# Optimization experiments

Measured on AMD Instinct MI355X. Metric: run time of the kernel, lower is better.

## Reference

```python
import jax, jax.numpy as jnp
import numpy as np

# Module constants (from init_kwargs)
P = 10000          # query points
G = 6400           # gaussians
C = 18             # semantic classes
H, W, D = 200, 200, 16
GRID = 0.5
SCALE_MULT = 3.0
PC_MIN = jnp.array([-50.0, -50.0, -5.0], dtype=jnp.float32)
COV_IDX = np.array([0, 4, 8, 1, 5, 2])  # xx, yy, zz, xy, yz, xz of flattened 3x3


def setup_inputs() -> dict:
    key = jax.random.key(0)
    k1, k2, k3, k4, k5, k6 = jax.random.split(key, 6)
    extent = jnp.array([H, W, D], jnp.float32) * GRID  # [100, 100, 8] meters
    eps = 1e-3  # keep strictly inside grid so int voxel coords are in-range
    pts = PC_MIN + jax.random.uniform(k1, (1, P, 3), jnp.float32) * (extent - eps)
    means3D = PC_MIN + jax.random.uniform(k2, (1, G, 3), jnp.float32) * (extent - eps)
    opacities = jax.random.uniform(k3, (1, G), jnp.float32)
    semantics = jax.random.normal(k4, (1, G, C), jnp.float32)
    # scales in [0.2, 1.0] m -> radii = ceil(max_scale*3/0.5) >= 2 (assert radii >= 1)
    scales = 0.2 + 0.8 * jax.random.uniform(k5, (1, G, 3), jnp.float32)
    # cov3D is the (symmetric PD) precision matrix: R diag(1/s^2) R^T
    A = jax.random.normal(k6, (1, G, 3, 3), jnp.float32)
    Q, _ = jnp.linalg.qr(A)
    inv_var = 1.0 / (scales ** 2)
    cov3D = jnp.einsum('bgij,bgj,bgkj->bgik', Q, inv_var, Q)
    return dict(pts=pts, means3D=means3D, opacities=opacities,
                semantics=semantics, scales=scales, cov3D=cov3D)


def reference(pts, means3D, opacities, semantics, scales, cov3D):
    # squeeze batch dim (module asserts batch == 1)
    p = pts[0]                     # [P,3]
    mu = means3D[0]                # [G,3]
    op = opacities[0]              # [G]
    sem = semantics[0]             # [G,C]
    sc = scales[0]                 # [G,3]
    cov = cov3D[0].reshape(G, 9)[:, COV_IDX]  # [G,6]: xx,yy,zz,xy,yz,xz

    # integer voxel coords (cast truncates; coords are non-negative in-range)
    p_int = ((p - PC_MIN) / GRID).astype(jnp.int32)                              # [P,3]
    m_int = ((jax.lax.stop_gradient(mu) - PC_MIN) / GRID).astype(jnp.int32)      # [G,3]
    radii = jnp.ceil(sc.max(-1) * SCALE_MULT / GRID).astype(jnp.int32)           # [G]

    # voxel-box test: point voxel within per-axis radius of gaussian voxel
    mask = (jnp.abs(p_int[:, None, :] - m_int[None, :, :]) <= radii[None, :, None]).all(-1)  # [P,G]

    # Mahalanobis power with precision matrix entries
    d = p[:, None, :] - mu[None, :, :]           # [P,G,3]
    dx, dy, dz = d[..., 0], d[..., 1], d[..., 2]
    power = (-0.5 * (cov[None, :, 0] * dx * dx
                     + cov[None, :, 1] * dy * dy
                     + cov[None, :, 2] * dz * dz)
             - cov[None, :, 3] * dx * dy
             - cov[None, :, 4] * dy * dz
             - cov[None, :, 5] * dx * dz)        # [P,G]

    w = jnp.where(mask, jnp.exp(power) * op[None, :], 0.0)  # [P,G]
    logits = w @ sem                                         # [P,C]
    return logits
```

## Files before the change

kernel.cpp:

```cpp
#include <hip/hip_runtime.h>
#include <math.h>

#define P_TOTAL 10000
#define G_TOTAL 6400
#define C_CLS   18
#define CS_SH   3
#define NCX     25
#define NCELL   (NCX * NCX)
#define BCAP    256
#define PCAP    96
#define NTHR    512

__global__ void __launch_bounds__(NTHR)
la_cell1(const float* __restrict__ pts,
         const float* __restrict__ means3D,
         const float* __restrict__ opacities,
         const float* __restrict__ semantics,
         const float* __restrict__ scales,
         const float* __restrict__ cov3D,
         float* __restrict__ out) {
    __shared__ int4 sbox[BCAP];
    __shared__ int  splist[PCAP];
    __shared__ int  snb, snp;

    const int t = threadIdx.x;
    const int cell = blockIdx.x;
    const int ccx = cell % NCX;
    const int ccy = cell / NCX;

    if (t == 0) { snb = 0; snp = 0; }
    __syncthreads();

    for (int i = t; i < P_TOTAL; i += NTHR) {
        float px = pts[i * 3 + 0];
        float py = pts[i * 3 + 1];
        int cx = ((int)((px + 50.0f) * 2.0f)) >> CS_SH;
        int cy = ((int)((py + 50.0f) * 2.0f)) >> CS_SH;
        if (cx == ccx && cy == ccy) {
            int s = atomicAdd(&snp, 1);
            if (s < PCAP) splist[s] = i;
        }
    }

    for (int g = t; g < G_TOTAL; g += NTHR) {
        float mx = means3D[g * 3 + 0];
        float my = means3D[g * 3 + 1];
        float mz = means3D[g * 3 + 2];
        float sx = scales[g * 3 + 0];
        float sy = scales[g * 3 + 1];
        float sz = scales[g * 3 + 2];
        int mix = (int)((mx + 50.0f) * 2.0f);
        int miy = (int)((my + 50.0f) * 2.0f);
        int miz = (int)((mz + 5.0f) * 2.0f);
        int r = (int)ceilf((fmaxf(fmaxf(sx, sy), sz) * 3.0f) * 2.0f);
        int w = 2 * r;
        int minx = mix - r, miny = miy - r, minz = miz - r;
        int cx0 = max(minx, 0) >> CS_SH;
        int cx1 = min(minx + w, 199) >> CS_SH;
        int cy0 = max(miny, 0) >> CS_SH;
        int cy1 = min(miny + w, 199) >> CS_SH;
        if (ccx >= cx0 && ccx <= cx1 && ccy >= cy0 && ccy <= cy1) {
            int s = atomicAdd(&snb, 1);
            if (s < BCAP) sbox[s] = make_int4(minx, miny, minz, (w << 16) | g);
        }
    }
    __syncthreads();

    const int np = min(snp, PCAP);
    const int nb = min(snb, BCAP);
    const int wv = t >> 6, lane = t & 63;

    for (int idx = wv; idx < np; idx += NTHR / 64) {
        int pt = splist[idx];
        float px = pts[pt * 3 + 0];
        float py = pts[pt * 3 + 1];
        float pz = pts[pt * 3 + 2];
        int pix = (int)((px + 50.0f) * 2.0f);
        int piy = (int)((py + 50.0f) * 2.0f);
        int piz = (int)((pz + 5.0f) * 2.0f);

        float acc = 0.0f;
        for (int base = 0; base < nb; base += 64) {
            int i = base + lane;
            float wgt = 0.0f;
            int gid = 0;
            if (i < nb) {
                int4 b = sbox[i];
                unsigned w  = ((unsigned)b.w) >> 16;
                unsigned ux = (unsigned)(pix - b.x);
                unsigned uy = (unsigned)(piy - b.y);
                unsigned uz = (unsigned)(piz - b.z);
                if (ux <= w && uy <= w && uz <= w) {
                    gid = b.w & 0xffff;
                    float mx = means3D[gid * 3 + 0];
                    float my = means3D[gid * 3 + 1];
                    float mz = means3D[gid * 3 + 2];
                    const float* cv = cov3D + (size_t)gid * 9;
                    float dx = px - mx, dy = py - my, dz = pz - mz;
                    float pw = -0.5f * (cv[0] * dx * dx + cv[4] * dy * dy + cv[8] * dz * dz)
                               - cv[1] * dx * dy - cv[5] * dy * dz - cv[2] * dx * dz;
                    wgt = __expf(pw) * opacities[gid];
                }
            }
            unsigned long long m = __ballot(wgt != 0.0f);
            while (m) {
                int h = (int)__builtin_ctzll(m);
                m &= m - 1;
                float wh = __shfl(wgt, h, 64);
                int   gh = __shfl(gid, h, 64);
                if (lane < C_CLS)
                    acc = fmaf(wh, semantics[(size_t)gh * C_CLS + lane], acc);
            }
        }

        if (lane < C_CLS)
            out[(size_t)pt * C_CLS + lane] = acc;
    }
}

extern "C" void kernel_launch(void* const* d_in, const int* in_sizes, int n_in,
                              void* d_out, int out_size, void* d_ws, size_t ws_size,
                              hipStream_t stream) {
    const float* pts      = (const float*)d_in[0];
    const float* means3D  = (const float*)d_in[1];
    const float* opac     = (const float*)d_in[2];
    const float* sem      = (const float*)d_in[3];
    const float* scales   = (const float*)d_in[4];
    const float* cov3D    = (const float*)d_in[5];
    float* out = (float*)d_out;

    la_cell1<<<NCELL, NTHR, 0, stream>>>(pts, means3D, opac, sem, scales, cov3D, out);
}
```

Baseline: 31.02 us.

## Bin points and gaussians globally once, with a grid-wide barrier before per-cell compute

Before this change, every block scanned all points and all gaussians to find the ones in its own cell. Now a single parallel pass bins points and gaussian footprints into per-cell lists in workspace using global atomics. A software grid barrier then separates binning from compute, and a persistent grid of 256 blocks loops over the 625 cells. The semantic accumulation also batches 16 ballot hits per pass to expose memory-level parallelism. The costs are a memset launch, global atomic contention, and a spin barrier that relies on all blocks being co-resident. PCAP also drops to 64, which could truncate points in dense cells.

```diff
diff --git a/kernel.cpp b/kernel.cpp
--- a/kernel.cpp
+++ b/kernel.cpp
@@ -7,42 +7,48 @@
 #define CS_SH   3
 #define NCX     25
 #define NCELL   (NCX * NCX)
-#define BCAP    256
-#define PCAP    96
-#define NTHR    512
+#define MAXE    256
+#define PCAP    64
+#define NBLK    256
+#define NTHR    256
+#define HB      16
 
-__global__ void __launch_bounds__(NTHR)
-la_cell1(const float* __restrict__ pts,
-         const float* __restrict__ means3D,
-         const float* __restrict__ opacities,
-         const float* __restrict__ semantics,
-         const float* __restrict__ scales,
-         const float* __restrict__ cov3D,
-         float* __restrict__ out) {
-    __shared__ int4 sbox[BCAP];
-    __shared__ int  splist[PCAP];
-    __shared__ int  snb, snp;
+#define OFF_BAR    0
+#define OFF_CNT    64
+#define OFF_PCNT   4096
+#define OFF_PLIST  8192
+#define OFF_ENT    (8192 + NCELL * PCAP * 4)
+
+__global__ void __launch_bounds__(NTHR, 4)
+la_bar(const float* __restrict__ pts,
+       const float* __restrict__ means3D,
+       const float* __restrict__ opacities,
+       const float* __restrict__ semantics,
+       const float* __restrict__ scales,
+       const float* __restrict__ cov3D,
+       char* __restrict__ ws,
+       float* __restrict__ out) {
+    int*  bar     = (int*)(ws + OFF_BAR);
+    int*  counts  = (int*)(ws + OFF_CNT);
+    int*  pcnt    = (int*)(ws + OFF_PCNT);
+    int*  plist   = (int*)(ws + OFF_PLIST);
+    int4* entries = (int4*)(ws + OFF_ENT);
 
     const int t = threadIdx.x;
-    const int cell = blockIdx.x;
-    const int ccx = cell % NCX;
-    const int ccy = cell / NCX;
+    const int gtid = blockIdx.x * NTHR + t;
 
-    if (t == 0) { snb = 0; snp = 0; }
-    __syncthreads();
-
-    for (int i = t; i < P_TOTAL; i += NTHR) {
-        float px = pts[i * 3 + 0];
-        float py = pts[i * 3 + 1];
+    if (gtid < P_TOTAL) {
+        float px = pts[gtid * 3 + 0];
+        float py = pts[gtid * 3 + 1];
         int cx = ((int)((px + 50.0f) * 2.0f)) >> CS_SH;
         int cy = ((int)((py + 50.0f) * 2.0f)) >> CS_SH;
-        if (cx == ccx && cy == ccy) {
-            int s = atomicAdd(&snp, 1);
-            if (s < PCAP) splist[s] = i;
-        }
+        int cell = cy * NCX + cx;
+        int s = atomicAdd(&pcnt[cell], 1);
+        if (s < PCAP) plist[cell * PCAP + s] = gtid;
     }
 
-    for (int g = t; g < G_TOTAL; g += NTHR) {
+    if (gtid < G_TOTAL) {
+        int g = gtid;
         float mx = means3D[g * 3 + 0];
         float my = means3D[g * 3 + 1];
         float mz = means3D[g * 3 + 2];
@@ -59,62 +65,95 @@
         int cx1 = min(minx + w, 199) >> CS_SH;
         int cy0 = max(miny, 0) >> CS_SH;
         int cy1 = min(miny + w, 199) >> CS_SH;
-        if (ccx >= cx0 && ccx <= cx1 && ccy >= cy0 && ccy <= cy1) {
-            int s = atomicAdd(&snb, 1);
-            if (s < BCAP) sbox[s] = make_int4(minx, miny, minz, (w << 16) | g);
+        int4 e = make_int4(minx, miny, minz, (w << 16) | g);
+        for (int cy = cy0; cy <= cy1; ++cy) {
+            for (int cx = cx0; cx <= cx1; ++cx) {
+                int cell = cy * NCX + cx;
+                int s = atomicAdd(&counts[cell], 1);
+                if (s < MAXE) entries[(size_t)cell * MAXE + s] = e;
+            }
         }
     }
+
+    __threadfence();
     __syncthreads();
+    if (t == 0) {
+        atomicAdd(&bar[0], 1);
+        while (atomicAdd(&bar[0], 0) < NBLK)
+            __builtin_amdgcn_s_sleep(8);
+    }
+    __syncthreads();
+    __threadfence();
 
-    const int np = min(snp, PCAP);
-    const int nb = min(snb, BCAP);
+    __shared__ int4 sbox[MAXE];
+    __shared__ int  spl[PCAP];
     const int wv = t >> 6, lane = t & 63;
 
-    for (int idx = wv; idx < np; idx += NTHR / 64) {
-        int pt = splist[idx];
-        float px = pts[pt * 3 + 0];
-        float py = pts[pt * 3 + 1];
-        float pz = pts[pt * 3 + 2];
-        int pix = (int)((px + 50.0f) * 2.0f);
-        int piy = (int)((py + 50.0f) * 2.0f);
-        int piz = (int)((pz + 5.0f) * 2.0f);
+    for (int cell = blockIdx.x; cell < NCELL; cell += NBLK) {
+        int nb = min(counts[cell], MAXE);
+        int np = min(pcnt[cell], PCAP);
+        __syncthreads();
+        for (int i = t; i < nb; i += NTHR) sbox[i] = entries[(size_t)cell * MAXE + i];
+        for (int i = t; i < np; i += NTHR) spl[i] = plist[cell * PCAP + i];
+        __syncthreads();
 
-        float acc = 0.0f;
-        for (int base = 0; base < nb; base += 64) {
-            int i = base + lane;
-            float wgt = 0.0f;
-            int gid = 0;
-            if (i < nb) {
-                int4 b = sbox[i];
-                unsigned w  = ((unsigned)b.w) >> 16;
-                unsigned ux = (unsigned)(pix - b.x);
-                unsigned uy = (unsigned)(piy - b.y);
-                unsigned uz = (unsigned)(piz - b.z);
-                if (ux <= w && uy <= w && uz <= w) {
-                    gid = b.w & 0xffff;
-                    float mx = means3D[gid * 3 + 0];
-                    float my = means3D[gid * 3 + 1];
-                    float mz = means3D[gid * 3 + 2];
-                    const float* cv = cov3D + (size_t)gid * 9;
-                    float dx = px - mx, dy = py - my, dz = pz - mz;
-                    float pw = -0.5f * (cv[0] * dx * dx + cv[4] * dy * dy + cv[8] * dz * dz)
-                               - cv[1] * dx * dy - cv[5] * dy * dz - cv[2] * dx * dz;
-                    wgt = __expf(pw) * opacities[gid];
+        for (int idx = wv; idx < np; idx += NTHR / 64) {
+            int pt = spl[idx];
+            float px = pts[pt * 3 + 0];
+            float py = pts[pt * 3 + 1];
+            float pz = pts[pt * 3 + 2];
+            int pix = (int)((px + 50.0f) * 2.0f);
+            int piy = (int)((py + 50.0f) * 2.0f);
+            int piz = (int)((pz + 5.0f) * 2.0f);
+
+            float acc = 0.0f;
+            for (int base = 0; base < nb; base += 64) {
+                int i = base + lane;
+                float wgt = 0.0f;
+                int gid = 0;
+                if (i < nb) {
+                    int4 b = sbox[i];
+                    unsigned w  = ((unsigned)b.w) >> 16;
+                    unsigned ux = (unsigned)(pix - b.x);
+                    unsigned uy = (unsigned)(piy - b.y);
+                    unsigned uz = (unsigned)(piz - b.z);
+                    if (ux <= w && uy <= w && uz <= w) {
+                        gid = b.w & 0xffff;
+                        float mx = means3D[gid * 3 + 0];
+                        float my = means3D[gid * 3 + 1];
+                        float mz = means3D[gid * 3 + 2];
+                        const float* cv = cov3D + (size_t)gid * 9;
+                        float dx = px - mx, dy = py - my, dz = pz - mz;
+                        float pw = -0.5f * (cv[0] * dx * dx + cv[4] * dy * dy + cv[8] * dz * dz)
+                                   - cv[1] * dx * dy - cv[5] * dy * dz - cv[2] * dx * dz;
+                        wgt = __expf(pw) * opacities[gid];
+                    }
+                }
+                unsigned long long m = __ballot(wgt != 0.0f);
+                while (m) {
+                    float wh[HB];
+                    int   gh[HB];
+#pragma unroll
+                    for (int k = 0; k < HB; ++k) {
+                        bool has = (m != 0);
+                        int h = (int)__builtin_ctzll(m | 0x8000000000000000ULL);
+                        float w_ = __shfl(wgt, h, 64);
+                        int   g_ = __shfl(gid, h, 64);
+                        wh[k] = has ? w_ : 0.0f;
+                        gh[k] = has ? g_ : 0;
+                        m &= m - 1;
+                    }
+                    if (lane < C_CLS) {
+#pragma unroll
+                        for (int k = 0; k < HB; ++k)
+                            acc = fmaf(wh[k], semantics[(size_t)gh[k] * C_CLS + lane], acc);
+                    }
                 }
             }
-            unsigned long long m = __ballot(wgt != 0.0f);
-            while (m) {
-                int h = (int)__builtin_ctzll(m);
-                m &= m - 1;
-                float wh = __shfl(wgt, h, 64);
-                int   gh = __shfl(gid, h, 64);
-                if (lane < C_CLS)
-                    acc = fmaf(wh, semantics[(size_t)gh * C_CLS + lane], acc);
-            }
+
+            if (lane < C_CLS)
+                out[(size_t)pt * C_CLS + lane] = acc;
         }
-
-        if (lane < C_CLS)
-            out[(size_t)pt * C_CLS + lane] = acc;
     }
 }
 
@@ -128,6 +167,8 @@
     const float* scales   = (const float*)d_in[4];
     const float* cov3D    = (const float*)d_in[5];
     float* out = (float*)d_out;
+    char* ws = (char*)d_ws;
 
-    la_cell1<<<NCELL, NTHR, 0, stream>>>(pts, means3D, opac, sem, scales, cov3D, out);
+    hipMemsetAsync(ws, 0, 8192, stream);
+    la_bar<<<NBLK, NTHR, 0, stream>>>(pts, means3D, opac, sem, scales, cov3D, ws, out);
 }
```

Result: slower. 97.24 us (+213.5%).

## Prebin gaussians and points into supercells before per-cell gather

Applied to the files above, without the earlier changes.

Replaces the per-block full scan over all 10000 points and 6400 gaussians with a three-kernel pipeline. The first kernel packs gaussian voxel boxes, the second scatters gaussians and points into 5x5 supercell lists in workspace, and the gather kernel reads only its supercell's candidates. It also batches the ballot-driven semantic accumulation into groups of 16 hits so the loads can be issued together. This adds two extra kernel launches and global atomics, plus fixed capacities (768 and 640 entries per supercell) that could silently drop entries if they overflow.

```diff
diff --git a/kernel.cpp b/kernel.cpp
--- a/kernel.cpp
+++ b/kernel.cpp
@@ -7,42 +7,28 @@
 #define CS_SH   3
 #define NCX     25
 #define NCELL   (NCX * NCX)
+#define SC_DIV  5
+#define NSC     25
+#define SBCAP   768
+#define SPCAP   640
 #define BCAP    256
 #define PCAP    96
 #define NTHR    512
-
-__global__ void __launch_bounds__(NTHR)
-la_cell1(const float* __restrict__ pts,
-         const float* __restrict__ means3D,
-         const float* __restrict__ opacities,
-         const float* __restrict__ semantics,
-         const float* __restrict__ scales,
-         const float* __restrict__ cov3D,
-         float* __restrict__ out) {
-    __shared__ int4 sbox[BCAP];
-    __shared__ int  splist[PCAP];
-    __shared__ int  snb, snp;
-
-    const int t = threadIdx.x;
-    const int cell = blockIdx.x;
-    const int ccx = cell % NCX;
-    const int ccy = cell / NCX;
-
-    if (t == 0) { snb = 0; snp = 0; }
-    __syncthreads();
-
-    for (int i = t; i < P_TOTAL; i += NTHR) {
-        float px = pts[i * 3 + 0];
-        float py = pts[i * 3 + 1];
-        int cx = ((int)((px + 50.0f) * 2.0f)) >> CS_SH;
-        int cy = ((int)((py + 50.0f) * 2.0f)) >> CS_SH;
-        if (cx == ccx && cy == ccy) {
-            int s = atomicAdd(&snp, 1);
-            if (s < PCAP) splist[s] = i;
-        }
-    }
-
-    for (int g = t; g < G_TOTAL; g += NTHR) {
+#define HB      16
+
+#define OFF_BOX  0
+#define OFF_CNT  102400
+#define OFF_SBL  102656
+#define OFF_SPL  179456
+
+__global__ void la_pack(const float* __restrict__ means3D,
+                        const float* __restrict__ scales,
+                        char* __restrict__ ws) {
+    int4* boxes = (int4*)(ws + OFF_BOX);
+    int*  cnt   = (int*)(ws + OFF_CNT);
+    int tid = blockIdx.x * 256 + threadIdx.x;
+    if (tid < G_TOTAL) {
+        int g = tid;
         float mx = means3D[g * 3 + 0];
         float my = means3D[g * 3 + 1];
         float mz = means3D[g * 3 + 2];
@@ -54,14 +40,99 @@
         int miz = (int)((mz + 5.0f) * 2.0f);
         int r = (int)ceilf((fmaxf(fmaxf(sx, sy), sz) * 3.0f) * 2.0f);
         int w = 2 * r;
-        int minx = mix - r, miny = miy - r, minz = miz - r;
-        int cx0 = max(minx, 0) >> CS_SH;
-        int cx1 = min(minx + w, 199) >> CS_SH;
-        int cy0 = max(miny, 0) >> CS_SH;
-        int cy1 = min(miny + w, 199) >> CS_SH;
+        boxes[g] = make_int4(mix - r, miy - r, miz - r, (w << 16) | g);
+    } else if (tid < G_TOTAL + 64) {
+        cnt[tid - G_TOTAL] = 0;
+    }
+}
+
+__global__ void la_scat(const float* __restrict__ pts,
+                        char* __restrict__ ws) {
+    const int4* boxes = (const int4*)(ws + OFF_BOX);
+    int* cnt    = (int*)(ws + OFF_CNT);
+    int* sblist = (int*)(ws + OFF_SBL);
+    int* splist = (int*)(ws + OFF_SPL);
+    int tid = blockIdx.x * 256 + threadIdx.x;
+    if (tid < G_TOTAL * 4) {
+        int g = tid >> 2, k = tid & 3;
+        int4 b = boxes[g];
+        int w = b.w >> 16;
+        int cx0 = max(b.x, 0) >> CS_SH;
+        int cx1 = min(b.x + w, 199) >> CS_SH;
+        int cy0 = max(b.y, 0) >> CS_SH;
+        int cy1 = min(b.y + w, 199) >> CS_SH;
+        int sx0 = cx0 / SC_DIV, sx1 = cx1 / SC_DIV;
+        int sy0 = cy0 / SC_DIV, sy1 = cy1 / SC_DIV;
+        int dx = k & 1, dy = k >> 1;
+        int sx = sx0 + dx, sy = sy0 + dy;
+        if (sx <= sx1 && sy <= sy1) {
+            int sc = sy * SC_DIV + sx;
+            int s = atomicAdd(&cnt[sc], 1);
+            if (s < SBCAP) sblist[sc * SBCAP + s] = g;
+        }
+    } else if (tid < G_TOTAL * 4 + P_TOTAL) {
+        int p = tid - G_TOTAL * 4;
+        float px = pts[p * 3 + 0];
+        float py = pts[p * 3 + 1];
+        int cx = ((int)((px + 50.0f) * 2.0f)) >> CS_SH;
+        int cy = ((int)((py + 50.0f) * 2.0f)) >> CS_SH;
+        int sc = (cy / SC_DIV) * SC_DIV + (cx / SC_DIV);
+        int s = atomicAdd(&cnt[32 + sc], 1);
+        if (s < SPCAP) splist[sc * SPCAP + s] = p;
+    }
+}
+
+__global__ void __launch_bounds__(NTHR)
+la_gather(const float* __restrict__ pts,
+          const float* __restrict__ means3D,
+          const float* __restrict__ opacities,
+          const float* __restrict__ semantics,
+          const float* __restrict__ cov3D,
+          const char* __restrict__ ws,
+          float* __restrict__ out) {
+    const int4* boxes  = (const int4*)(ws + OFF_BOX);
+    const int*  cnt    = (const int*)(ws + OFF_CNT);
+    const int*  sblist = (const int*)(ws + OFF_SBL);
+    const int*  splist = (const int*)(ws + OFF_SPL);
+
+    __shared__ int4 sbox[BCAP];
+    __shared__ int  spl[PCAP];
+    __shared__ int  snb, snp;
+
+    const int t = threadIdx.x;
+    const int cell = blockIdx.x;
+    const int ccx = cell % NCX;
+    const int ccy = cell / NCX;
+    const int sc  = (ccy / SC_DIV) * SC_DIV + (ccx / SC_DIV);
+
+    if (t == 0) { snb = 0; snp = 0; }
+    __syncthreads();
+
+    const int npl = min(cnt[32 + sc], SPCAP);
+    for (int i = t; i < npl; i += NTHR) {
+        int p = splist[sc * SPCAP + i];
+        float px = pts[p * 3 + 0];
+        float py = pts[p * 3 + 1];
+        int cx = ((int)((px + 50.0f) * 2.0f)) >> CS_SH;
+        int cy = ((int)((py + 50.0f) * 2.0f)) >> CS_SH;
+        if (cx == ccx && cy == ccy) {
+            int s = atomicAdd(&snp, 1);
+            if (s < PCAP) spl[s] = p;
+        }
+    }
+
+    const int nbl = min(cnt[sc], SBCAP);
+    for (int i = t; i < nbl; i += NTHR) {
+        int g = sblist[sc * SBCAP + i];
+        int4 b = boxes[g];
+        int w = b.w >> 16;
+        int cx0 = max(b.x, 0) >> CS_SH;
+        int cx1 = min(b.x + w, 199) >> CS_SH;
+        int cy0 = max(b.y, 0) >> CS_SH;
+        int cy1 = min(b.y + w, 199) >> CS_SH;
         if (ccx >= cx0 && ccx <= cx1 && ccy >= cy0 && ccy <= cy1) {
             int s = atomicAdd(&snb, 1);
-            if (s < BCAP) sbox[s] = make_int4(minx, miny, minz, (w << 16) | g);
+            if (s < BCAP) sbox[s] = b;
         }
     }
     __syncthreads();
@@ -71,7 +142,7 @@
     const int wv = t >> 6, lane = t & 63;
 
     for (int idx = wv; idx < np; idx += NTHR / 64) {
-        int pt = splist[idx];
+        int pt = spl[idx];
         float px = pts[pt * 3 + 0];
         float py = pts[pt * 3 + 1];
         float pz = pts[pt * 3 + 2];
@@ -104,12 +175,23 @@
             }
             unsigned long long m = __ballot(wgt != 0.0f);
             while (m) {
-                int h = (int)__builtin_ctzll(m);
-                m &= m - 1;
-                float wh = __shfl(wgt, h, 64);
-                int   gh = __shfl(gid, h, 64);
-                if (lane < C_CLS)
-                    acc = fmaf(wh, semantics[(size_t)gh * C_CLS + lane], acc);
+                float wh[HB];
+                int   gh[HB];
+#pragma unroll
+                for (int k = 0; k < HB; ++k) {
+                    bool has = (m != 0);
+                    int h = (int)__builtin_ctzll(m | 0x8000000000000000ULL);
+                    float w_ = __shfl(wgt, h, 64);
+                    int   g_ = __shfl(gid, h, 64);
+                    wh[k] = has ? w_ : 0.0f;
+                    gh[k] = has ? g_ : 0;
+                    m &= m - 1;
+                }
+                if (lane < C_CLS) {
+#pragma unroll
+                    for (int k = 0; k < HB; ++k)
+                        acc = fmaf(wh[k], semantics[(size_t)gh[k] * C_CLS + lane], acc);
+                }
             }
         }
 
@@ -128,6 +210,9 @@
     const float* scales   = (const float*)d_in[4];
     const float* cov3D    = (const float*)d_in[5];
     float* out = (float*)d_out;
-
-    la_cell1<<<NCELL, NTHR, 0, stream>>>(pts, means3D, opac, sem, scales, cov3D, out);
-}
+    char* ws = (char*)d_ws;
+
+    la_pack<<<(G_TOTAL + 64 + 255) / 256, 256, 0, stream>>>(means3D, scales, ws);
+    la_scat<<<(G_TOTAL * 4 + P_TOTAL + 255) / 256, 256, 0, stream>>>(pts, ws);
+    la_gather<<<NCELL, NTHR, 0, stream>>>(pts, means3D, opac, sem, cov3D, ws, out);
+}
```

New measurement: 61.88 us. +99.5%, slower.
